# Kernel optimization log

Measured on AMD Instinct MI355X. Metric: run time of the kernel, lower is better.

The kernel has to match this reference:

```python
import jax, jax.numpy as jnp
import numpy as np


def _pairwise_dist(p, t):
    # p: [B, N, 3], t: [B, M, 3] -> Euclidean distances [B, N, M]
    # ||p - t||^2 = ||p||^2 + ||t||^2 - 2 p.t  (avoids [B,N,M,3] intermediate)
    p2 = jnp.sum(p * p, axis=-1)  # [B, N]
    t2 = jnp.sum(t * t, axis=-1)  # [B, M]
    cross = jnp.einsum('bnd,bmd->bnm', p, t)  # [B, N, M]
    d2 = p2[:, :, None] + t2[:, None, :] - 2.0 * cross
    return jnp.sqrt(jnp.maximum(d2, 0.0))


def setup_inputs() -> dict:
    key = jax.random.key(0)
    k1, k2 = jax.random.split(key)
    pred = jax.random.normal(k1, (4, 3, 8192), dtype=jnp.float32)
    target = jax.random.normal(k2, (4, 3, 8192), dtype=jnp.float32)
    return {"pred": pred, "target": target}


def reference(pred, target):
    # pred, target: [B, 3, N] channel-first point clouds
    p = jnp.swapaxes(pred, 2, 1)    # [B, N, 3]
    t = jnp.swapaxes(target, 2, 1)  # [B, M, 3]
    dist = _pairwise_dist(p, t)     # [B, N, M]
    min_p_to_t = jnp.min(dist, axis=2).mean()
    min_t_to_p = jnp.min(dist, axis=1).mean()
    return min_p_to_t + min_t_to_p
```

## Files before the change

kernel.cpp:

```cpp
#include <hip/hip_runtime.h>


typedef __attribute__((ext_vector_type(8)))  short bf16x8;
typedef __attribute__((ext_vector_type(16))) float f32x16;

constexpr int NPTS    = 8192;
constexpr int BATCH   = 4;
constexpr int NB_ROWS = 128;
constexpr int N_NB    = NPTS / NB_ROWS;
constexpr int STEPS   = NPTS / 32;

constexpr size_t TBL_BYTES = (size_t)BATCH * NPTS * 32;

__device__ inline unsigned short f2bf(float x) {
    unsigned u = __float_as_uint(x);
    u += 0x7FFFu + ((u >> 16) & 1u);
    return (unsigned short)(u >> 16);
}
__device__ inline float bf2f(unsigned short h) {
    return __uint_as_float(((unsigned)h) << 16);
}

__global__ __launch_bounds__(256) void pack_both(
    const float* __restrict__ pred, const float* __restrict__ targ,
    unsigned int* __restrict__ wsb) {
    int tid = blockIdx.x * 256 + threadIdx.x;
    int which = tid >> 15;
    int r = tid & 32767;
    int b = r >> 13, m = r & (NPTS - 1);
    const float* src = which ? pred : targ;
    const float* tb = src + (size_t)b * 3 * NPTS;
    float tx = tb[m], ty = tb[NPTS + m], tz = tb[2 * NPTS + m];
    float t2 = fmaf(tx, tx, fmaf(ty, ty, tz * tz));
    unsigned short xh = f2bf(tx), yh = f2bf(ty), zh = f2bf(tz);
    unsigned short xl = f2bf(tx - bf2f(xh));
    unsigned short yl = f2bf(ty - bf2f(yh));
    unsigned short zl = f2bf(tz - bf2f(zh));
    unsigned short t2h = f2bf(t2), t2l = f2bf(t2 - bf2f(t2h));
    const unsigned short ONE = 0x3F80;
    unsigned int u0 = (unsigned)ONE | ((unsigned)ONE << 16);
    unsigned int u1 = (unsigned)t2h | ((unsigned)t2l << 16);
    unsigned int u2 = (unsigned)xh  | ((unsigned)xl  << 16);
    unsigned int u3 = (unsigned)xh  | ((unsigned)yh  << 16);
    unsigned int u4 = (unsigned)yl  | ((unsigned)yh  << 16);
    unsigned int u5 = (unsigned)zh  | ((unsigned)zl  << 16);
    unsigned int u6 = (unsigned)zh;
    uint4* dst = (uint4*)wsb;
    dst[(size_t)tid * 2]     = make_uint4(u0, u1, u2, u3);
    dst[(size_t)tid * 2 + 1] = make_uint4(u4, u5, u6, 0u);
}

__global__ __launch_bounds__(256) void chamfer_both(
    const float* __restrict__ pred, const float* __restrict__ targ,
    const unsigned int* __restrict__ wsb, float* __restrict__ out) {
    const int tid  = threadIdx.x;
    const int lane = tid & 63;
    const int wv   = tid >> 6;
    const int nb   = blockIdx.x;
    const int dir  = blockIdx.y;
    const int b    = blockIdx.z;

    const float* rowsrc = dir ? targ : pred;
    const int row = nb * NB_ROWS + wv * 32 + (lane & 31);
    const int g   = lane >> 5;
    const float* pb = rowsrc + (size_t)b * 3 * NPTS;
    float px = pb[row], py = pb[NPTS + row], pz = pb[2 * NPTS + row];
    float p2 = fmaf(px, px, fmaf(py, py, pz * pz));
    unsigned short xh = f2bf(px), yh = f2bf(py), zh = f2bf(pz);
    unsigned short xl = f2bf(px - bf2f(xh));
    unsigned short yl = f2bf(py - bf2f(yh));
    unsigned short zl = f2bf(pz - bf2f(zh));
    unsigned short p2h = f2bf(p2), p2l = f2bf(p2 - bf2f(p2h));
    unsigned short mxh = f2bf(-2.f * bf2f(xh)), mxl = f2bf(-2.f * bf2f(xl));
    unsigned short myh = f2bf(-2.f * bf2f(yh)), myl = f2bf(-2.f * bf2f(yl));
    unsigned short mzh = f2bf(-2.f * bf2f(zh)), mzl = f2bf(-2.f * bf2f(zl));
    const unsigned short ONE = 0x3F80;
    unsigned short av[8];
    if (g == 0) {
        av[0]=p2h; av[1]=p2l; av[2]=ONE; av[3]=ONE;
        av[4]=mxh; av[5]=mxh; av[6]=mxl; av[7]=myh;
    } else {
        av[0]=myh; av[1]=myl; av[2]=mzh; av[3]=mzh;
        av[4]=mzl; av[5]=0;   av[6]=0;   av[7]=0;
    }
    bf16x8 af;
    #pragma unroll
    for (int i = 0; i < 8; ++i) af[i] = (short)av[i];

    f32x16 zero;
    #pragma unroll
    for (int i = 0; i < 16; ++i) zero[i] = 0.f;

    float racc[16];
    #pragma unroll
    for (int i = 0; i < 16; ++i) racc[i] = __int_as_float(0x7F800000);

    const char* btab = (const char*)wsb
        + (size_t)dir * TBL_BYTES
        + (size_t)b * NPTS * 32
        + (size_t)(lane & 31) * 32 + (size_t)g * 16;

    auto ldg = [&](int s) -> bf16x8 {
        return *reinterpret_cast<const bf16x8*>(btab + (size_t)s * 1024);
    };
    auto step2 = [&](bf16x8 f0, bf16x8 f1) {
        f32x16 c0 = __builtin_amdgcn_mfma_f32_32x32x16_bf16(af, f0, zero, 0, 0, 0);
        f32x16 c1 = __builtin_amdgcn_mfma_f32_32x32x16_bf16(af, f1, zero, 0, 0, 0);
        #pragma unroll
        for (int i = 0; i < 16; ++i)
            racc[i] = fminf(fminf(racc[i], c0[i]), c1[i]);
    };

    bf16x8 f0 = ldg(0), f1 = ldg(1), f2 = ldg(2), f3 = ldg(3);
    for (int s = 0; s < STEPS - 4; s += 4) {
        bf16x8 n0 = ldg(s + 4), n1 = ldg(s + 5), n2 = ldg(s + 6), n3 = ldg(s + 7);
        step2(f0, f1);
        step2(f2, f3);
        f0 = n0; f1 = n1; f2 = n2; f3 = n3;
    }
    step2(f0, f1);
    step2(f2, f3);

    float s = 0.f;
    #pragma unroll
    for (int i = 0; i < 16; ++i) {
        float v = racc[i];
        v = fminf(v, __shfl_xor(v, 1));
        v = fminf(v, __shfl_xor(v, 2));
        v = fminf(v, __shfl_xor(v, 4));
        v = fminf(v, __shfl_xor(v, 8));
        v = fminf(v, __shfl_xor(v, 16));
        s += sqrtf(fmaxf(v, 0.f));
    }
    s += __shfl_xor(s, 32);

    __shared__ float wsum[4];
    if (lane == 0) wsum[wv] = s;
    __syncthreads();
    if (tid == 0)
        atomicAdd(out, (wsum[0] + wsum[1] + wsum[2] + wsum[3]) * (1.0f / 32768.0f));
}

extern "C" void kernel_launch(void* const* d_in, const int* in_sizes, int n_in,
                              void* d_out, int out_size, void* d_ws, size_t ws_size,
                              hipStream_t stream) {
    const float* pred = (const float*)d_in[0];
    const float* targ = (const float*)d_in[1];
    float* out = (float*)d_out;
    unsigned int* wsb = (unsigned int*)d_ws;

    hipMemsetAsync(d_out, 0, sizeof(float), stream);

    pack_both<<<(2 * BATCH * NPTS) / 256, 256, 0, stream>>>(pred, targ, wsb);

    dim3 grid(N_NB, 2, BATCH);
    chamfer_both<<<grid, 256, 0, stream>>>(pred, targ, wsb, out);
}
```

Before: 90.55 us.

## Split column range across blocks and reuse B fragments across two row tiles

```diff
diff --git a/kernel.cpp b/kernel.cpp
--- a/kernel.cpp
+++ b/kernel.cpp
@@ -4,13 +4,16 @@
 typedef __attribute__((ext_vector_type(8)))  short bf16x8;
 typedef __attribute__((ext_vector_type(16))) float f32x16;
 
-constexpr int NPTS    = 8192;
-constexpr int BATCH   = 4;
-constexpr int NB_ROWS = 128;
-constexpr int N_NB    = NPTS / NB_ROWS;
-constexpr int STEPS   = NPTS / 32;
+constexpr int NPTS   = 8192;
+constexpr int BATCH  = 4;
+constexpr int CSPLIT = 4;
+constexpr int CCOLS  = NPTS / CSPLIT;
+constexpr int RT     = 64;
+constexpr int N_RT   = NPTS / RT;
+constexpr int STEPS  = CCOLS / 32;
 
 constexpr size_t TBL_BYTES = (size_t)BATCH * NPTS * 32;
+constexpr size_t ROW_OFF   = 2 * TBL_BYTES;
 
 __device__ inline unsigned short f2bf(float x) {
     unsigned u = __float_as_uint(x);
@@ -50,95 +53,135 @@
     dst[(size_t)tid * 2 + 1] = make_uint4(u4, u5, u6, 0u);
 }
 
-__global__ __launch_bounds__(256) void chamfer_both(
+__global__ __launch_bounds__(64) void chamfer_v2(
     const float* __restrict__ pred, const float* __restrict__ targ,
-    const unsigned int* __restrict__ wsb, float* __restrict__ out) {
-    const int tid  = threadIdx.x;
-    const int lane = tid & 63;
-    const int wv   = tid >> 6;
-    const int nb   = blockIdx.x;
-    const int dir  = blockIdx.y;
-    const int b    = blockIdx.z;
+    const unsigned int* __restrict__ wsb, float* __restrict__ ws_row) {
+    const int lane = threadIdx.x;
+    const int g    = lane >> 5;
+    const int rt   = blockIdx.x;
+    const int cs   = blockIdx.y;
+    const int db   = blockIdx.z;
+    const int dir  = db & 1;
+    const int b    = db >> 1;
 
     const float* rowsrc = dir ? targ : pred;
-    const int row = nb * NB_ROWS + wv * 32 + (lane & 31);
-    const int g   = lane >> 5;
     const float* pb = rowsrc + (size_t)b * 3 * NPTS;
-    float px = pb[row], py = pb[NPTS + row], pz = pb[2 * NPTS + row];
-    float p2 = fmaf(px, px, fmaf(py, py, pz * pz));
-    unsigned short xh = f2bf(px), yh = f2bf(py), zh = f2bf(pz);
-    unsigned short xl = f2bf(px - bf2f(xh));
-    unsigned short yl = f2bf(py - bf2f(yh));
-    unsigned short zl = f2bf(pz - bf2f(zh));
-    unsigned short p2h = f2bf(p2), p2l = f2bf(p2 - bf2f(p2h));
-    unsigned short mxh = f2bf(-2.f * bf2f(xh)), mxl = f2bf(-2.f * bf2f(xl));
-    unsigned short myh = f2bf(-2.f * bf2f(yh)), myl = f2bf(-2.f * bf2f(yl));
-    unsigned short mzh = f2bf(-2.f * bf2f(zh)), mzl = f2bf(-2.f * bf2f(zl));
+
     const unsigned short ONE = 0x3F80;
-    unsigned short av[8];
-    if (g == 0) {
-        av[0]=p2h; av[1]=p2l; av[2]=ONE; av[3]=ONE;
-        av[4]=mxh; av[5]=mxh; av[6]=mxl; av[7]=myh;
-    } else {
-        av[0]=myh; av[1]=myl; av[2]=mzh; av[3]=mzh;
-        av[4]=mzl; av[5]=0;   av[6]=0;   av[7]=0;
-    }
-    bf16x8 af;
-    #pragma unroll
-    for (int i = 0; i < 8; ++i) af[i] = (short)av[i];
+    auto build_af = [&](int row) -> bf16x8 {
+        float px = pb[row], py = pb[NPTS + row], pz = pb[2 * NPTS + row];
+        float p2 = fmaf(px, px, fmaf(py, py, pz * pz));
+        unsigned short xh = f2bf(px), yh = f2bf(py), zh = f2bf(pz);
+        unsigned short xl = f2bf(px - bf2f(xh));
+        unsigned short yl = f2bf(py - bf2f(yh));
+        unsigned short zl = f2bf(pz - bf2f(zh));
+        unsigned short p2h = f2bf(p2), p2l = f2bf(p2 - bf2f(p2h));
+        unsigned short mxh = f2bf(-2.f * bf2f(xh)), mxl = f2bf(-2.f * bf2f(xl));
+        unsigned short myh = f2bf(-2.f * bf2f(yh)), myl = f2bf(-2.f * bf2f(yl));
+        unsigned short mzh = f2bf(-2.f * bf2f(zh)), mzl = f2bf(-2.f * bf2f(zl));
+        unsigned short av[8];
+        if (g == 0) {
+            av[0]=p2h; av[1]=p2l; av[2]=ONE; av[3]=ONE;
+            av[4]=mxh; av[5]=mxh; av[6]=mxl; av[7]=myh;
+        } else {
+            av[0]=myh; av[1]=myl; av[2]=mzh; av[3]=mzh;
+            av[4]=mzl; av[5]=0;   av[6]=0;   av[7]=0;
+        }
+        bf16x8 f;
+        #pragma unroll
+        for (int i = 0; i < 8; ++i) f[i] = (short)av[i];
+        return f;
+    };
+
+    const int r0 = rt * RT + (lane & 31);
+    bf16x8 af0 = build_af(r0);
+    bf16x8 af1 = build_af(r0 + 32);
 
     f32x16 zero;
     #pragma unroll
     for (int i = 0; i < 16; ++i) zero[i] = 0.f;
 
-    float racc[16];
-    #pragma unroll
-    for (int i = 0; i < 16; ++i) racc[i] = __int_as_float(0x7F800000);
+    float racc0[16], racc1[16];
+    #pragma unroll
+    for (int i = 0; i < 16; ++i) {
+        racc0[i] = __int_as_float(0x7F800000);
+        racc1[i] = __int_as_float(0x7F800000);
+    }
 
     const char* btab = (const char*)wsb
         + (size_t)dir * TBL_BYTES
         + (size_t)b * NPTS * 32
+        + (size_t)cs * CCOLS * 32
         + (size_t)(lane & 31) * 32 + (size_t)g * 16;
 
     auto ldg = [&](int s) -> bf16x8 {
         return *reinterpret_cast<const bf16x8*>(btab + (size_t)s * 1024);
     };
-    auto step2 = [&](bf16x8 f0, bf16x8 f1) {
-        f32x16 c0 = __builtin_amdgcn_mfma_f32_32x32x16_bf16(af, f0, zero, 0, 0, 0);
-        f32x16 c1 = __builtin_amdgcn_mfma_f32_32x32x16_bf16(af, f1, zero, 0, 0, 0);
+    auto proc2 = [&](bf16x8 fa, bf16x8 fb) {
+        f32x16 ca = __builtin_amdgcn_mfma_f32_32x32x16_bf16(af0, fa, zero, 0, 0, 0);
+        f32x16 cb = __builtin_amdgcn_mfma_f32_32x32x16_bf16(af0, fb, zero, 0, 0, 0);
         #pragma unroll
         for (int i = 0; i < 16; ++i)
-            racc[i] = fminf(fminf(racc[i], c0[i]), c1[i]);
+            racc0[i] = fminf(fminf(racc0[i], ca[i]), cb[i]);
+        f32x16 cc = __builtin_amdgcn_mfma_f32_32x32x16_bf16(af1, fa, zero, 0, 0, 0);
+        f32x16 cd = __builtin_amdgcn_mfma_f32_32x32x16_bf16(af1, fb, zero, 0, 0, 0);
+        #pragma unroll
+        for (int i = 0; i < 16; ++i)
+            racc1[i] = fminf(fminf(racc1[i], cc[i]), cd[i]);
     };
 
-    bf16x8 f0 = ldg(0), f1 = ldg(1), f2 = ldg(2), f3 = ldg(3);
-    for (int s = 0; s < STEPS - 4; s += 4) {
-        bf16x8 n0 = ldg(s + 4), n1 = ldg(s + 5), n2 = ldg(s + 6), n3 = ldg(s + 7);
-        step2(f0, f1);
-        step2(f2, f3);
-        f0 = n0; f1 = n1; f2 = n2; f3 = n3;
-    }
-    step2(f0, f1);
-    step2(f2, f3);
-
-    float s = 0.f;
+    bf16x8 f0 = ldg(0), f1 = ldg(1);
+    for (int s = 0; s < STEPS - 2; s += 2) {
+        bf16x8 n0 = ldg(s + 2), n1 = ldg(s + 3);
+        proc2(f0, f1);
+        f0 = n0; f1 = n1;
+    }
+    proc2(f0, f1);
+
     #pragma unroll
     for (int i = 0; i < 16; ++i) {
-        float v = racc[i];
+        float v = racc0[i];
         v = fminf(v, __shfl_xor(v, 1));
         v = fminf(v, __shfl_xor(v, 2));
         v = fminf(v, __shfl_xor(v, 4));
         v = fminf(v, __shfl_xor(v, 8));
         v = fminf(v, __shfl_xor(v, 16));
-        s += sqrtf(fmaxf(v, 0.f));
-    }
-    s += __shfl_xor(s, 32);
-
+        racc0[i] = v;
+        float w = racc1[i];
+        w = fminf(w, __shfl_xor(w, 1));
+        w = fminf(w, __shfl_xor(w, 2));
+        w = fminf(w, __shfl_xor(w, 4));
+        w = fminf(w, __shfl_xor(w, 8));
+        w = fminf(w, __shfl_xor(w, 16));
+        racc1[i] = w;
+    }
+    if ((lane & 31) == 0) {
+        float* base = ws_row + ((size_t)db * CSPLIT + cs) * NPTS + (size_t)rt * RT;
+        #pragma unroll
+        for (int i = 0; i < 16; ++i) {
+            int r = (i & 3) + 8 * (i >> 2) + 4 * g;
+            base[r]      = racc0[i];
+            base[32 + r] = racc1[i];
+        }
+    }
+}
+
+__global__ __launch_bounds__(256) void reduce_rows(
+    const float* __restrict__ ws_row, float* __restrict__ out) {
+    int tid = blockIdx.x * 256 + threadIdx.x;
+    int db  = tid >> 13;
+    int row = tid & (NPTS - 1);
+    const float* base = ws_row + (size_t)db * CSPLIT * NPTS + row;
+    float v = base[0];
+    #pragma unroll
+    for (int cshift = 1; cshift < CSPLIT; ++cshift)
+        v = fminf(v, base[(size_t)cshift * NPTS]);
+    float d = sqrtf(fmaxf(v, 0.f)) * (1.0f / 32768.0f);
+    for (int off = 32; off; off >>= 1) d += __shfl_down(d, off);
     __shared__ float wsum[4];
-    if (lane == 0) wsum[wv] = s;
+    if ((threadIdx.x & 63) == 0) wsum[threadIdx.x >> 6] = d;
     __syncthreads();
-    if (tid == 0)
-        atomicAdd(out, (wsum[0] + wsum[1] + wsum[2] + wsum[3]) * (1.0f / 32768.0f));
+    if (threadIdx.x == 0) atomicAdd(out, wsum[0] + wsum[1] + wsum[2] + wsum[3]);
 }
 
 extern "C" void kernel_launch(void* const* d_in, const int* in_sizes, int n_in,
@@ -147,12 +190,16 @@
     const float* pred = (const float*)d_in[0];
     const float* targ = (const float*)d_in[1];
     float* out = (float*)d_out;
-    unsigned int* wsb = (unsigned int*)d_ws;
+    char* ws = (char*)d_ws;
+    unsigned int* wsb = (unsigned int*)ws;
+    float* ws_row = (float*)(ws + ROW_OFF);
 
     hipMemsetAsync(d_out, 0, sizeof(float), stream);
 
     pack_both<<<(2 * BATCH * NPTS) / 256, 256, 0, stream>>>(pred, targ, wsb);
 
-    dim3 grid(N_NB, 2, BATCH);
-    chamfer_both<<<grid, 256, 0, stream>>>(pred, targ, wsb, out);
-}
+    dim3 grid(N_RT, CSPLIT, 2 * BATCH);
+    chamfer_v2<<<grid, 64, 0, stream>>>(pred, targ, wsb, ws_row);
+
+    reduce_rows<<<(2 * BATCH * NPTS) / 256, 256, 0, stream>>>(ws_row, out);
+}
```

New measurement: 93.55 us. 3.3% more time.
